# Kernel optimization log

Hardware: AMD Instinct MI355X
Metric: run time of the kernel (lower is better)

The kernel has to match this reference:

```python
import jax, jax.numpy as jnp
import numpy as np

N, FEAT, N_ANC, ANC = 131072, 256, 64, 128
EPS = 1e-5

def _xavier(key, shape, gain=1.414):
    fan_in, fan_out = shape[0], shape[1]
    a = gain * np.sqrt(6.0 / (fan_in + fan_out))
    return jax.random.uniform(key, shape, jnp.float32, -a, a)

def setup_inputs() -> dict:
    key = jax.random.key(0)
    ks = jax.random.split(key, 6)
    return {
        "features": jax.random.normal(ks[0], (N, FEAT), jnp.float32),
        "W_send": _xavier(ks[1], (FEAT, ANC)),            # send_attention.weight_matrix
        "a_send": _xavier(ks[2], (2 * ANC, 1)),           # send_attention.attention_vector
        "W_recv": _xavier(ks[3], (N_ANC, FEAT)),          # receive_attention.weight_matrix
        "a_recv": _xavier(ks[4], (2 * FEAT, 1)),          # receive_attention.attention_vector
        "anchors": _xavier(ks[5], (N_ANC, ANC), gain=1.0),# anchor_embeddings
        "g_feat": jnp.ones((FEAT,), jnp.float32),
        "b_feat": jnp.zeros((FEAT,), jnp.float32),
        "g_anc": jnp.ones((N_ANC,), jnp.float32),
        "b_anc": jnp.zeros((N_ANC,), jnp.float32),
    }

def _layer_norm(x, g, b):
    mu = jnp.mean(x, axis=-1, keepdims=True)
    var = jnp.mean((x - mu) ** 2, axis=-1, keepdims=True)  # biased, as in torch LN
    return (x - mu) * jax.lax.rsqrt(var + EPS) * g + b

def _fca(x, W, a):
    # Original: scores_ij = cat(h_i, h_j) @ a = (h_i @ a1) + (h_j @ a2);
    # softmax over j of (s1_i + s2_j) == softmax(s2)_j, independent of i.
    # attended_i = sum_j softmax(s2)_j * h_j  -> same row broadcast to all i.
    H = x @ W                      # [N, D]
    D = W.shape[1]
    s2 = H @ a[D:, 0]              # [N]
    w = jax.nn.softmax(s2)         # [N]
    pooled = w @ H                 # [D]
    return jnp.broadcast_to(pooled, (x.shape[0], D))

def reference(features, W_send, a_send, W_recv, a_recv, anchors, g_feat, b_feat, g_anc, b_anc):
    nf = _layer_norm(features, g_feat, b_feat)      # [N, FEAT]
    sent = _fca(nf, W_send, a_send)                 # [N, ANC]
    proj = sent @ anchors.T                         # [N, N_ANC]
    na = _layer_norm(proj, g_anc, b_anc)            # [N, N_ANC]
    recv = _fca(na, W_recv, a_recv)                 # [N, FEAT]
    return features + jnp.sin(recv)
```

## Files before the change

### kernel.cpp

```cpp
#include <hip/hip_runtime.h>
#include <hip/hip_bf16.h>

#define N_ROWS 131072
#define FEAT   256
#define N_ANC  64
#define ANC    128
#define LN_EPS 1e-5f

#define WPB    4
#define GMAX   64

__device__ __forceinline__ float bf2f(unsigned short u) {
    return __uint_as_float(((unsigned int)u) << 16);
}
__device__ __forceinline__ unsigned short f2bf(float f) {
    unsigned int u = __float_as_uint(f);
    u += 0x7fffu + ((u >> 16) & 1u);
    return (unsigned short)(u >> 16);
}

__device__ __forceinline__ bool is_bf16(const void* g_feat) {
    return *(const unsigned int*)g_feat != 0x3F800000u;
}

template<bool BF>
__device__ __forceinline__ float ld1(const void* p, int i) {
    return BF ? bf2f(((const unsigned short*)p)[i]) : ((const float*)p)[i];
}

template<bool BF>
__device__ __forceinline__ void ld4row(const void* feat, size_t row, int lane, float x[4]) {
    if (BF) {
        ushort4 w = *(const ushort4*)((const unsigned short*)feat + row * FEAT + lane * 4);
        x[0] = bf2f(w.x); x[1] = bf2f(w.y); x[2] = bf2f(w.z); x[3] = bf2f(w.w);
    } else {
        float4 w = *(const float4*)((const float*)feat + row * FEAT + lane * 4);
        x[0] = w.x; x[1] = w.y; x[2] = w.z; x[3] = w.w;
    }
}

template<bool BF>
__device__ __forceinline__ void k0_body(
    const void* Wsend, const void* a_send, float* v)
{
    __shared__ float a2[ANC];
    int t = threadIdx.x;
    if (t < ANC) a2[t] = ld1<BF>(a_send, ANC + t);
    __syncthreads();
    float acc = 0.f;
    #pragma unroll 4
    for (int j = 0; j < ANC; ++j) acc = fmaf(ld1<BF>(Wsend, t * ANC + j), a2[j], acc);
    v[t] = acc;
}

__global__ __launch_bounds__(256) void k0_vvec(
    const void* __restrict__ Wsend, const void* __restrict__ a_send,
    const void* __restrict__ g_feat, float* __restrict__ v)
{
    if (is_bf16(g_feat)) k0_body<true>(Wsend, a_send, v);
    else                 k0_body<false>(Wsend, a_send, v);
}

template<bool BF>
__device__ __forceinline__ void k1_body(
    const void* feat, const void* g_feat, const void* b_feat, const float* v,
    float* pm, float* pd, float* pu, int nwave, int npair)
{
    const int tid  = threadIdx.x;
    const int lane = tid & 63;
    const int w    = tid >> 6;
    const int gw   = blockIdx.x * WPB + w;

    float g[4], b[4], gv[4];
    float sgv = 0.f, sbv = 0.f;
    #pragma unroll
    for (int j = 0; j < 4; ++j) {
        float vg = ld1<BF>(g_feat, lane * 4 + j);
        float vb = ld1<BF>(b_feat, lane * 4 + j);
        float vv = v[lane * 4 + j];
        g[j] = vg; b[j] = vb;
        gv[j] = vg * vv;
        sgv += gv[j];
        sbv += vb * vv;
    }
    #pragma unroll
    for (int off = 1; off < 64; off <<= 1) {
        sgv += __shfl_xor(sgv, off, 64);
        sbv += __shfl_xor(sbv, off, 64);
    }

    float m = -1e30f, d = 0.f;
    float u[4] = {0.f, 0.f, 0.f, 0.f};

    for (int it = 0; it < npair; ++it) {
        const size_t ra = (size_t)gw + (size_t)(it * 2) * nwave;
        const size_t rb = ra + nwave;
        float xa[4], xb[4];
        ld4row<BF>(feat, ra, lane, xa);
        ld4row<BF>(feat, rb, lane, xb);

        float sA = 0.f, qA = 0.f, dA = 0.f;
        float sB = 0.f, qB = 0.f, dB = 0.f;
        #pragma unroll
        for (int j = 0; j < 4; ++j) {
            sA += xa[j]; qA = fmaf(xa[j], xa[j], qA); dA = fmaf(xa[j], gv[j], dA);
            sB += xb[j]; qB = fmaf(xb[j], xb[j], qB); dB = fmaf(xb[j], gv[j], dB);
        }
        #pragma unroll
        for (int off = 1; off < 64; off <<= 1) {
            sA += __shfl_xor(sA, off, 64);
            qA += __shfl_xor(qA, off, 64);
            dA += __shfl_xor(dA, off, 64);
            sB += __shfl_xor(sB, off, 64);
            qB += __shfl_xor(qB, off, 64);
            dB += __shfl_xor(dB, off, 64);
        }
        const float muA = sA * (1.f / 256.f);
        const float muB = sB * (1.f / 256.f);
        const float rA  = rsqrtf(fmaf(-muA, muA, qA * (1.f / 256.f)) + LN_EPS);
        const float rB  = rsqrtf(fmaf(-muB, muB, qB * (1.f / 256.f)) + LN_EPS);
        const float s2A = fmaf(rA, fmaf(-muA, sgv, dA), sbv);
        const float s2B = fmaf(rB, fmaf(-muB, sgv, dB), sbv);

        float nfa[4], nfb[4];
        #pragma unroll
        for (int j = 0; j < 4; ++j) {
            nfa[j] = fmaf((xa[j] - muA) * rA, g[j], b[j]);
            nfb[j] = fmaf((xb[j] - muB) * rB, g[j], b[j]);
        }

        const float mx = fmaxf(m, fmaxf(s2A, s2B));
        const float sc = __expf(m - mx);
        const float ea = __expf(s2A - mx);
        const float eb = __expf(s2B - mx);
        d = fmaf(d, sc, ea + eb);
        #pragma unroll
        for (int j = 0; j < 4; ++j)
            u[j] = fmaf(u[j], sc, fmaf(ea, nfa[j], eb * nfb[j]));
        m = mx;
    }

    __shared__ float su[WPB][FEAT];
    __shared__ float smd[WPB][2];
    #pragma unroll
    for (int j = 0; j < 4; ++j) su[w][lane * 4 + j] = u[j];
    if (lane == 0) { smd[w][0] = m; smd[w][1] = d; }
    __syncthreads();

    const float M  = fmaxf(fmaxf(smd[0][0], smd[1][0]), fmaxf(smd[2][0], smd[3][0]));
    const float e0 = __expf(smd[0][0] - M);
    const float e1 = __expf(smd[1][0] - M);
    const float e2 = __expf(smd[2][0] - M);
    const float e3 = __expf(smd[3][0] - M);
    if (tid == 0) {
        pm[blockIdx.x] = M;
        pd[blockIdx.x] = smd[0][1] * e0 + smd[1][1] * e1 + smd[2][1] * e2 + smd[3][1] * e3;
    }
    pu[blockIdx.x * FEAT + tid] =
        su[0][tid] * e0 + su[1][tid] * e1 + su[2][tid] * e2 + su[3][tid] * e3;
}

__global__ __launch_bounds__(256) void k1_pass(
    const void* __restrict__ feat,
    const void* __restrict__ g_feat,
    const void* __restrict__ b_feat,
    const float* __restrict__ v,
    float* __restrict__ pm, float* __restrict__ pd, float* __restrict__ pu,
    int nwave, int npair)
{
    if (is_bf16(g_feat)) k1_body<true >(feat, g_feat, b_feat, v, pm, pd, pu, nwave, npair);
    else                 k1_body<false>(feat, g_feat, b_feat, v, pm, pd, pu, nwave, npair);
}

__global__ __launch_bounds__(256) void k2a_reduce(
    const float* __restrict__ pm, const float* __restrict__ pd,
    const float* __restrict__ pu,
    float* __restrict__ qm, float* __restrict__ qd, float* __restrict__ qu,
    int Q)
{
    const int tid  = threadIdx.x;
    const int g    = blockIdx.x;
    const int base = g * Q;

    __shared__ float sm[GMAX];
    __shared__ float se[GMAX];

    if (tid < Q) sm[tid] = pm[base + tid];
    __syncthreads();

    float M = -1e30f;
    #pragma unroll 16
    for (int i = 0; i < Q; ++i) M = fmaxf(M, sm[i]);
    __syncthreads();

    if (tid < Q) se[tid] = __expf(sm[tid] - M);
    __syncthreads();

    if (tid == 0) {
        float dsum = 0.f;
        for (int i = 0; i < Q; ++i) dsum = fmaf(pd[base + i], se[i], dsum);
        qd[g] = dsum;
        qm[g] = M;
    }

    float acc = 0.f;
    #pragma unroll 16
    for (int i = 0; i < Q; ++i)
        acc = fmaf(pu[(size_t)(base + i) * FEAT + tid], se[i], acc);
    qu[g * FEAT + tid] = acc;
}

template<bool BF>
__device__ __forceinline__ void k2_body(
    const float* pm, const float* pd, const float* pu,
    const void* Wsend, const void* anchors, const void* Wrecv,
    const void* g_anc, const void* b_anc, float* sv, int P)
{
    const int tid  = threadIdx.x;
    const int lane = tid & 63;
    const int wv   = tid >> 6;

    __shared__ float sE[GMAX];
    __shared__ float sred[4];
    __shared__ float sun[FEAT];
    __shared__ float spool[ANC];
    __shared__ float sproj[N_ANC];
    __shared__ float sna[N_ANC];
    __shared__ float sc2[2];

    float mm = -1e30f;
    for (int i = tid; i < P; i += 256) mm = fmaxf(mm, pm[i]);
    #pragma unroll
    for (int off = 1; off < 64; off <<= 1) mm = fmaxf(mm, __shfl_xor(mm, off, 64));
    if (lane == 0) sred[wv] = mm;
    __syncthreads();
    const float M = fmaxf(fmaxf(sred[0], sred[1]), fmaxf(sred[2], sred[3]));

    float dt = 0.f;
    for (int i = tid; i < P; i += 256) {
        const float e = __expf(pm[i] - M);
        sE[i] = e;
        dt = fmaf(pd[i], e, dt);
    }
    #pragma unroll
    for (int off = 1; off < 64; off <<= 1) dt += __shfl_xor(dt, off, 64);
    __syncthreads();
    if (lane == 0) sred[wv] = dt;
    __syncthreads();
    const float D = (sred[0] + sred[1]) + (sred[2] + sred[3]);

    float acc = 0.f;
    #pragma unroll 16
    for (int bb = 0; bb < P; ++bb) acc = fmaf(pu[bb * FEAT + tid], sE[bb], acc);
    sun[tid] = acc / D;
    __syncthreads();

    if (tid < ANC) {
        float p = 0.f;
        #pragma unroll 4
        for (int k = 0; k < FEAT; ++k) p = fmaf(sun[k], ld1<BF>(Wsend, k * ANC + tid), p);
        spool[tid] = p;
    }
    __syncthreads();

    if (tid < N_ANC) {
        float p = 0.f;
        #pragma unroll 4
        for (int j = 0; j < ANC; ++j) p = fmaf(spool[j], ld1<BF>(anchors, tid * ANC + j), p);
        sproj[tid] = p;
    }
    __syncthreads();

    if (tid == 0) {
        float s = 0.f, q = 0.f;
        for (int k = 0; k < N_ANC; ++k) { s += sproj[k]; q = fmaf(sproj[k], sproj[k], q); }
        const float mu  = s * (1.f / 64.f);
        const float var = q * (1.f / 64.f) - mu * mu;
        sc2[0] = mu; sc2[1] = rsqrtf(var + LN_EPS);
    }
    __syncthreads();
    if (tid < N_ANC)
        sna[tid] = fmaf((sproj[tid] - sc2[0]) * sc2[1], ld1<BF>(g_anc, tid), ld1<BF>(b_anc, tid));
    __syncthreads();

    {
        float h = 0.f;
        #pragma unroll 4
        for (int k = 0; k < N_ANC; ++k) h = fmaf(sna[k], ld1<BF>(Wrecv, k * FEAT + tid), h);
        sv[tid] = sinf(h);
    }
}

__global__ __launch_bounds__(256) void k2_combine(
    const float* __restrict__ pm, const float* __restrict__ pd,
    const float* __restrict__ pu,
    const void* __restrict__ Wsend, const void* __restrict__ anchors,
    const void* __restrict__ Wrecv, const void* __restrict__ g_anc,
    const void* __restrict__ b_anc, const void* __restrict__ g_feat,
    float* __restrict__ sv, int P)
{
    if (is_bf16(g_feat)) k2_body<true >(pm, pd, pu, Wsend, anchors, Wrecv, g_anc, b_anc, sv, P);
    else                 k2_body<false>(pm, pd, pu, Wsend, anchors, Wrecv, g_anc, b_anc, sv, P);
}

__global__ __launch_bounds__(256) void k3_out(
    const void* __restrict__ feat, const float* __restrict__ sv,
    const void* __restrict__ g_feat, void* __restrict__ out)
{
    const int tid = threadIdx.x;
    const int stride = gridDim.x * blockDim.x;

    if (is_bf16(g_feat)) {
        const int c = (tid * 8) & 255;
        float s[8];
        #pragma unroll
        for (int j = 0; j < 8; ++j) s[j] = sv[c + j];
        const int total8 = N_ROWS * FEAT / 8;
        for (int i = blockIdx.x * blockDim.x + tid; i < total8; i += stride) {
            uint4 w = ((const uint4*)feat)[i];
            unsigned int in[4] = {w.x, w.y, w.z, w.w};
            unsigned int r[4];
            #pragma unroll
            for (int j = 0; j < 4; ++j) {
                const float lo = bf2f((unsigned short)(in[j] & 0xffffu));
                const float hi = bf2f((unsigned short)(in[j] >> 16));
                const unsigned short ol = f2bf(lo + s[j * 2]);
                const unsigned short oh = f2bf(hi + s[j * 2 + 1]);
                r[j] = (unsigned int)ol | ((unsigned int)oh << 16);
            }
            uint4 o; o.x = r[0]; o.y = r[1]; o.z = r[2]; o.w = r[3];
            ((uint4*)out)[i] = o;
        }
    } else {
        const int c = (tid * 4) & 255;
        float s[4];
        #pragma unroll
        for (int j = 0; j < 4; ++j) s[j] = sv[c + j];
        const int total4 = N_ROWS * FEAT / 4;
        for (int i = blockIdx.x * blockDim.x + tid; i < total4; i += stride) {
            float4 w = ((const float4*)feat)[i];
            float4 o;
            o.x = w.x + s[0]; o.y = w.y + s[1];
            o.z = w.z + s[2]; o.w = w.w + s[3];
            ((float4*)out)[i] = o;
        }
    }
}

extern "C" void kernel_launch(void* const* d_in, const int* in_sizes, int n_in,
                              void* d_out, int out_size, void* d_ws, size_t ws_size,
                              hipStream_t stream)
{
    const void* feat    = d_in[0];
    const void* Wsend   = d_in[1];
    const void* a_send  = d_in[2];
    const void* Wrecv   = d_in[3];
    const void* anchors = d_in[5];
    const void* g_feat  = d_in[6];
    const void* b_feat  = d_in[7];
    const void* g_anc   = d_in[8];
    const void* b_anc   = d_in[9];

    int P = 1024;
    while (P > 1 &&
           (size_t)(2048 + 1032 * (size_t)P + 1032 * GMAX) > ws_size) P >>= 1;
    const int G = (P >= GMAX) ? GMAX : P;
    const int Q = P / G;

    const int nwave = P * WPB;
    const int npair = N_ROWS / (2 * nwave);

    float* ws = (float*)d_ws;
    float* v  = ws;
    float* sv = ws + 256;
    float* pm = ws + 512;
    float* pd = ws + 512 + P;
    float* pu = ws + 512 + 2 * P;
    float* qm = pu + (size_t)P * FEAT;
    float* qd = qm + G;
    float* qu = qd + G;

    k0_vvec<<<1, 256, 0, stream>>>(Wsend, a_send, g_feat, v);
    k1_pass<<<P, 256, 0, stream>>>(feat, g_feat, b_feat, v, pm, pd, pu, nwave, npair);
    k2a_reduce<<<G, 256, 0, stream>>>(pm, pd, pu, qm, qd, qu, Q);
    k2_combine<<<1, 256, 0, stream>>>(qm, qd, qu, Wsend, anchors, Wrecv,
                                      g_anc, b_anc, g_feat, sv, G);
    k3_out<<<4096, 256, 0, stream>>>(feat, sv, g_feat, d_out);
}
```

Before: 308.1 us.

## Defer LN affine to combine, double partial blocks, nontemporal output stream

```diff
diff --git a/kernel.cpp b/kernel.cpp
--- a/kernel.cpp
+++ b/kernel.cpp
@@ -9,6 +9,9 @@
 
 #define WPB    4
 #define GMAX   64
+
+typedef unsigned int u32x4 __attribute__((ext_vector_type(4)));
+typedef float        f32x4 __attribute__((ext_vector_type(4)));
 
 __device__ __forceinline__ float bf2f(unsigned short u) {
     return __uint_as_float(((unsigned int)u) << 16);
@@ -71,14 +74,13 @@
     const int w    = tid >> 6;
     const int gw   = blockIdx.x * WPB + w;
 
-    float g[4], b[4], gv[4];
+    float gv[4];
     float sgv = 0.f, sbv = 0.f;
     #pragma unroll
     for (int j = 0; j < 4; ++j) {
-        float vg = ld1<BF>(g_feat, lane * 4 + j);
-        float vb = ld1<BF>(b_feat, lane * 4 + j);
-        float vv = v[lane * 4 + j];
-        g[j] = vg; b[j] = vb;
+        const float vg = ld1<BF>(g_feat, lane * 4 + j);
+        const float vb = ld1<BF>(b_feat, lane * 4 + j);
+        const float vv = v[lane * 4 + j];
         gv[j] = vg * vv;
         sgv += gv[j];
         sbv += vb * vv;
@@ -122,21 +124,19 @@
         const float s2A = fmaf(rA, fmaf(-muA, sgv, dA), sbv);
         const float s2B = fmaf(rB, fmaf(-muB, sgv, dB), sbv);
 
-        float nfa[4], nfb[4];
-        #pragma unroll
-        for (int j = 0; j < 4; ++j) {
-            nfa[j] = fmaf((xa[j] - muA) * rA, g[j], b[j]);
-            nfb[j] = fmaf((xb[j] - muB) * rB, g[j], b[j]);
-        }
-
         const float mx = fmaxf(m, fmaxf(s2A, s2B));
         const float sc = __expf(m - mx);
         const float ea = __expf(s2A - mx);
         const float eb = __expf(s2B - mx);
         d = fmaf(d, sc, ea + eb);
-        #pragma unroll
-        for (int j = 0; j < 4; ++j)
-            u[j] = fmaf(u[j], sc, fmaf(ea, nfa[j], eb * nfb[j]));
+        const float cA = muA * rA;
+        const float cB = muB * rB;
+        #pragma unroll
+        for (int j = 0; j < 4; ++j) {
+            const float na = fmaf(xa[j], rA, -cA);
+            const float nb = fmaf(xb[j], rB, -cB);
+            u[j] = fmaf(u[j], sc, fmaf(ea, na, eb * nb));
+        }
         m = mx;
     }
 
@@ -184,12 +184,13 @@
 
     __shared__ float sm[GMAX];
     __shared__ float se[GMAX];
-
-    if (tid < Q) sm[tid] = pm[base + tid];
+    __shared__ float spd[GMAX];
+
+    if (tid < Q) { sm[tid] = pm[base + tid]; spd[tid] = pd[base + tid]; }
     __syncthreads();
 
     float M = -1e30f;
-    #pragma unroll 16
+    #pragma unroll 8
     for (int i = 0; i < Q; ++i) M = fmaxf(M, sm[i]);
     __syncthreads();
 
@@ -198,7 +199,7 @@
 
     if (tid == 0) {
         float dsum = 0.f;
-        for (int i = 0; i < Q; ++i) dsum = fmaf(pd[base + i], se[i], dsum);
+        for (int i = 0; i < Q; ++i) dsum = fmaf(spd[i], se[i], dsum);
         qd[g] = dsum;
         qm[g] = M;
     }
@@ -214,7 +215,8 @@
 __device__ __forceinline__ void k2_body(
     const float* pm, const float* pd, const float* pu,
     const void* Wsend, const void* anchors, const void* Wrecv,
-    const void* g_anc, const void* b_anc, float* sv, int P)
+    const void* g_anc, const void* b_anc,
+    const void* g_feat, const void* b_feat, float* sv, int P)
 {
     const int tid  = threadIdx.x;
     const int lane = tid & 63;
@@ -252,7 +254,7 @@
     float acc = 0.f;
     #pragma unroll 16
     for (int bb = 0; bb < P; ++bb) acc = fmaf(pu[bb * FEAT + tid], sE[bb], acc);
-    sun[tid] = acc / D;
+    sun[tid] = fmaf(ld1<BF>(g_feat, tid), acc / D, ld1<BF>(b_feat, tid));
     __syncthreads();
 
     if (tid < ANC) {
@@ -297,10 +299,12 @@
     const void* __restrict__ Wsend, const void* __restrict__ anchors,
     const void* __restrict__ Wrecv, const void* __restrict__ g_anc,
     const void* __restrict__ b_anc, const void* __restrict__ g_feat,
-    float* __restrict__ sv, int P)
-{
-    if (is_bf16(g_feat)) k2_body<true >(pm, pd, pu, Wsend, anchors, Wrecv, g_anc, b_anc, sv, P);
-    else                 k2_body<false>(pm, pd, pu, Wsend, anchors, Wrecv, g_anc, b_anc, sv, P);
+    const void* __restrict__ b_feat, float* __restrict__ sv, int P)
+{
+    if (is_bf16(g_feat))
+        k2_body<true >(pm, pd, pu, Wsend, anchors, Wrecv, g_anc, b_anc, g_feat, b_feat, sv, P);
+    else
+        k2_body<false>(pm, pd, pu, Wsend, anchors, Wrecv, g_anc, b_anc, g_feat, b_feat, sv, P);
 }
 
 __global__ __launch_bounds__(256) void k3_out(
@@ -317,19 +321,18 @@
         for (int j = 0; j < 8; ++j) s[j] = sv[c + j];
         const int total8 = N_ROWS * FEAT / 8;
         for (int i = blockIdx.x * blockDim.x + tid; i < total8; i += stride) {
-            uint4 w = ((const uint4*)feat)[i];
-            unsigned int in[4] = {w.x, w.y, w.z, w.w};
-            unsigned int r[4];
+            const u32x4 w = __builtin_nontemporal_load(&((const u32x4*)feat)[i]);
+            u32x4 o;
             #pragma unroll
             for (int j = 0; j < 4; ++j) {
-                const float lo = bf2f((unsigned short)(in[j] & 0xffffu));
-                const float hi = bf2f((unsigned short)(in[j] >> 16));
+                const unsigned int wj = w[j];
+                const float lo = bf2f((unsigned short)(wj & 0xffffu));
+                const float hi = bf2f((unsigned short)(wj >> 16));
                 const unsigned short ol = f2bf(lo + s[j * 2]);
                 const unsigned short oh = f2bf(hi + s[j * 2 + 1]);
-                r[j] = (unsigned int)ol | ((unsigned int)oh << 16);
+                o[j] = (unsigned int)ol | ((unsigned int)oh << 16);
             }
-            uint4 o; o.x = r[0]; o.y = r[1]; o.z = r[2]; o.w = r[3];
-            ((uint4*)out)[i] = o;
+            __builtin_nontemporal_store(o, &((u32x4*)out)[i]);
         }
     } else {
         const int c = (tid * 4) & 255;
@@ -338,11 +341,11 @@
         for (int j = 0; j < 4; ++j) s[j] = sv[c + j];
         const int total4 = N_ROWS * FEAT / 4;
         for (int i = blockIdx.x * blockDim.x + tid; i < total4; i += stride) {
-            float4 w = ((const float4*)feat)[i];
-            float4 o;
+            const f32x4 w = __builtin_nontemporal_load(&((const f32x4*)feat)[i]);
+            f32x4 o;
             o.x = w.x + s[0]; o.y = w.y + s[1];
             o.z = w.z + s[2]; o.w = w.w + s[3];
-            ((float4*)out)[i] = o;
+            __builtin_nontemporal_store(o, &((f32x4*)out)[i]);
         }
     }
 }
@@ -361,7 +364,7 @@
     const void* g_anc   = d_in[8];
     const void* b_anc   = d_in[9];
 
-    int P = 1024;
+    int P = 2048;
     while (P > 1 &&
            (size_t)(2048 + 1032 * (size_t)P + 1032 * GMAX) > ws_size) P >>= 1;
     const int G = (P >= GMAX) ? GMAX : P;
@@ -384,6 +387,6 @@
     k1_pass<<<P, 256, 0, stream>>>(feat, g_feat, b_feat, v, pm, pd, pu, nwave, npair);
     k2a_reduce<<<G, 256, 0, stream>>>(pm, pd, pu, qm, qd, qu, Q);
     k2_combine<<<1, 256, 0, stream>>>(qm, qd, qu, Wsend, anchors, Wrecv,
-                                      g_anc, b_anc, g_feat, sv, G);
+                                      g_anc, b_anc, g_feat, b_feat, sv, G);
     k3_out<<<4096, 256, 0, stream>>>(feat, sv, g_feat, d_out);
 }
```

Result: no change. 313.3 us (+1.7%).
